# Kernel optimization log

Measured on AMD Instinct MI355X. Metric: run time of the kernel, lower is better.

The kernel has to match this reference:

```python
import jax, jax.numpy as jnp
import numpy as np

DIM = 1024
N_HEADS = 16
HEAD_DIM = DIM // N_HEADS


def setup_inputs() -> dict:
    key = jax.random.key(0)
    ks = jax.random.split(key, 6)
    s = DIM ** -0.5
    return {
        "x": jax.random.normal(ks[0], (2, 2048, DIM), dtype=jnp.float32),
        "Wq": jax.random.normal(ks[1], (DIM, DIM), dtype=jnp.float32) * s,
        "Wk": jax.random.normal(ks[2], (DIM, DIM), dtype=jnp.float32) * s,
        "Wv": jax.random.normal(ks[3], (DIM, DIM), dtype=jnp.float32) * s,
        "Wo": jax.random.normal(ks[4], (DIM, DIM), dtype=jnp.float32) * s,
        "bo": jax.random.normal(ks[5], (DIM,), dtype=jnp.float32) * 0.01,
    }


def reference(x, Wq, Wk, Wv, Wo, bo):
    B, T, C = x.shape
    H, D = N_HEADS, HEAD_DIM
    # Linear(dim, dim, bias=False): y = x @ W^T
    q = (x @ Wq.T).reshape(B, T, H, D).transpose(0, 2, 1, 3)  # B H T D
    k = (x @ Wk.T).reshape(B, T, H, D).transpose(0, 2, 1, 3)
    v = (x @ Wv.T).reshape(B, T, H, D).transpose(0, 2, 1, 3)
    q = q * (D ** -0.5)
    attn = jnp.einsum('bhqd,bhkd->bhqk', q, k)  # B H T T
    causal_mask = jnp.triu(jnp.ones((T, T), dtype=bool), k=1)
    attn = jnp.where(causal_mask, -jnp.inf, attn)
    attn = jax.nn.softmax(attn, axis=-1)
    out = jnp.einsum('bhqk,bhkd->bhqd', attn, v)  # B H T D
    out = out.transpose(0, 2, 1, 3).reshape(B, T, C)
    return out @ Wo.T + bo
```

## Files before the change

kernel.cpp:

```cpp
#include <hip/hip_runtime.h>
#include <math.h>

typedef __attribute__((ext_vector_type(8))) short bf16x8;
typedef __attribute__((ext_vector_type(4))) float f32x4;
typedef __attribute__((ext_vector_type(16))) float f32x16;

__device__ __forceinline__ ushort f2bf(float f) {
  union { float f; unsigned u; } v; v.f = f;
  return (ushort)((v.u + 0x8000u) >> 16);
}

__device__ __forceinline__ void g2l16(const void* g, void* l) {
  __builtin_amdgcn_global_load_lds((const __attribute__((address_space(1))) unsigned*)g,
                                   (__attribute__((address_space(3))) unsigned*)l, 16, 0, 0);
}

__global__ __launch_bounds__(256) void cast_all(const float* __restrict__ x,
                                                const float* __restrict__ Wq,
                                                const float* __restrict__ Wk,
                                                const float* __restrict__ Wv,
                                                const float* __restrict__ Wo,
                                                ushort* __restrict__ xbf,
                                                ushort* __restrict__ wcat,
                                                float4* __restrict__ O32) {
  int i = blockIdx.x * 256 + threadIdx.x;
  if (i < 1048576) {
    float4 v = ((const float4*)x)[i];
    ushort4 u; u.x = f2bf(v.x); u.y = f2bf(v.y); u.z = f2bf(v.z); u.w = f2bf(v.w);
    ((ushort4*)xbf)[i] = u;
  } else if (i < 2097152) {
    int j = i - 1048576;
    int sel = j >> 18;
    const float* src = (sel == 0) ? Wq : (sel == 1) ? Wk : (sel == 2) ? Wv : Wo;
    float scale = (sel == 0) ? 0.125f * 1.44269504088896f : 1.0f;
    float4 v = ((const float4*)src)[j & 0x3FFFF];
    ushort4 u;
    u.x = f2bf(v.x * scale); u.y = f2bf(v.y * scale);
    u.z = f2bf(v.z * scale); u.w = f2bf(v.w * scale);
    ((ushort4*)wcat)[j] = u;
  } else {
    O32[i - 2097152] = float4{0.f, 0.f, 0.f, 0.f};
  }
}

__global__ __launch_bounds__(256) void gemm_qkv(const ushort* __restrict__ A,
                                                const ushort* __restrict__ B,
                                                ushort* __restrict__ C3,
                                                ushort* __restrict__ Vt) {
  const int K = 1024;
  __shared__ __align__(16) ushort smem[17408];
  ushort* As = smem;
  ushort* Bs = smem + 8192;
  const int m0 = blockIdx.y * 128, n0 = blockIdx.x * 128;
  const int tid = threadIdx.x, lane = tid & 63, wid = tid >> 6;
  const int quad = lane >> 4, lc = lane & 15;
  const int lrow = lane >> 2, lcol = (lane & 3) * 8;
  const int wm = (wid >> 1) * 64, wn = (wid & 1) * 64;

  f32x4 acc[4][4] = {};

  auto stage = [&](int k0, int nb) {
    const ushort* Ag = A + (size_t)(m0 + wid * 32 + lrow) * K + k0 + lcol;
    g2l16(Ag, &As[nb * 4096 + wid * 1024]);
    g2l16(Ag + (size_t)16 * K, &As[nb * 4096 + wid * 1024 + 512]);
    const ushort* Bg = B + (size_t)(n0 + wid * 32 + lrow) * K + k0 + lcol;
    g2l16(Bg, &Bs[nb * 4096 + wid * 1024]);
    g2l16(Bg + (size_t)16 * K, &Bs[nb * 4096 + wid * 1024 + 512]);
  };

  stage(0, 0);
  for (int k0 = 0; k0 < K; k0 += 32) {
    const int nb = (k0 >> 5) & 1;
    __syncthreads();
    if (k0 + 32 < K) stage(k0 + 32, nb ^ 1);

    bf16x8 af[4], bfr[4];
#pragma unroll
    for (int t = 0; t < 4; t++)
      af[t] = *(const bf16x8*)&As[nb * 4096 + (wm + t * 16 + lc) * 32 + quad * 8];
#pragma unroll
    for (int t = 0; t < 4; t++)
      bfr[t] = *(const bf16x8*)&Bs[nb * 4096 + (wn + t * 16 + lc) * 32 + quad * 8];
#pragma unroll
    for (int mt = 0; mt < 4; mt++)
#pragma unroll
      for (int nt = 0; nt < 4; nt++)
        acc[mt][nt] = __builtin_amdgcn_mfma_f32_16x16x32_bf16(af[mt], bfr[nt], acc[mt][nt], 0, 0, 0);
  }

  const int sel = n0 >> 10;
  if (sel < 2) {
#pragma unroll
    for (int mt = 0; mt < 4; mt++) {
#pragma unroll
      for (int r = 0; r < 4; r++) {
        int row = m0 + wm + mt * 16 + quad * 4 + r;
#pragma unroll
        for (int nt = 0; nt < 4; nt++) {
          int col = n0 + wn + nt * 16 + lc;
          size_t dst = ((size_t)sel << 22) + (size_t)row * 1024 + (col & 1023);
          C3[dst] = f2bf(acc[mt][nt][r]);
        }
      }
    }
  } else {
    __syncthreads();
#pragma unroll
    for (int mt = 0; mt < 4; mt++)
#pragma unroll
      for (int r = 0; r < 4; r++) {
        int tl = wm + mt * 16 + quad * 4 + r;
#pragma unroll
        for (int nt = 0; nt < 4; nt++)
          smem[(wn + nt * 16 + lc) * 136 + tl] = f2bf(acc[mt][nt][r]);
      }
    __syncthreads();
    const int hd0 = n0 - 2048, b = m0 >> 11, t_base = m0 & 2047;
#pragma unroll
    for (int i = 0; i < 8; i++) {
      int idx = i * 256 + tid;
      int dl = idx >> 4, tc = (idx & 15) * 8;
      uint4 v = *(const uint4*)&smem[dl * 136 + tc];
      int hd = hd0 + dl;
      *(uint4*)(Vt + (size_t)(b * 16 + (hd >> 6)) * 131072 +
                (size_t)(hd & 63) * 2048 + t_base + tc) = v;
    }
  }
}

__global__ __launch_bounds__(256) void gemm_proj(const ushort* __restrict__ A,
                                                 const ushort* __restrict__ B,
                                                 float* __restrict__ C,
                                                 const float* __restrict__ bias) {
  const int K = 1024;
  __shared__ __align__(16) ushort As[2][2][128 * 32];
  __shared__ __align__(16) ushort Bs[2][2][64 * 32];
  const int m0 = blockIdx.y * 128, n0 = blockIdx.x * 64;
  const int tid = threadIdx.x, lane = tid & 63, wid = tid >> 6;
  const int quad = lane >> 4, lc = lane & 15;
  const int lrow = lane >> 2, lcol = (lane & 3) * 8;
  const int wm = (wid >> 1) * 64, wn = (wid & 1) * 32;

  f32x4 acc[4][2] = {};

  auto stage = [&](int k0, int nb) {
    const ushort* Ag = A + (size_t)(m0 + wid * 32 + lrow) * K + k0 + lcol;
    g2l16(Ag,                       &As[nb][0][wid * 1024]);
    g2l16(Ag + (size_t)16 * K,      &As[nb][0][wid * 1024 + 512]);
    g2l16(Ag + 32,                  &As[nb][1][wid * 1024]);
    g2l16(Ag + (size_t)16 * K + 32, &As[nb][1][wid * 1024 + 512]);
    const ushort* Bg = B + (size_t)(n0 + wid * 16 + lrow) * K + k0 + lcol;
    g2l16(Bg,      &Bs[nb][0][wid * 512]);
    g2l16(Bg + 32, &Bs[nb][1][wid * 512]);
  };

  stage(0, 0);
  for (int k0 = 0; k0 < K; k0 += 64) {
    const int nb = (k0 >> 6) & 1;
    __syncthreads();
    if (k0 + 64 < K) stage(k0 + 64, nb ^ 1);

#pragma unroll
    for (int ks = 0; ks < 2; ks++) {
      bf16x8 af[4], bfr[2];
#pragma unroll
      for (int t = 0; t < 4; t++)
        af[t] = *(const bf16x8*)&As[nb][ks][(wm + t * 16 + lc) * 32 + quad * 8];
#pragma unroll
      for (int t = 0; t < 2; t++)
        bfr[t] = *(const bf16x8*)&Bs[nb][ks][(wn + t * 16 + lc) * 32 + quad * 8];
#pragma unroll
      for (int mt = 0; mt < 4; mt++)
#pragma unroll
        for (int nt = 0; nt < 2; nt++)
          acc[mt][nt] = __builtin_amdgcn_mfma_f32_16x16x32_bf16(af[mt], bfr[nt], acc[mt][nt], 0, 0, 0);
    }
  }

#pragma unroll
  for (int mt = 0; mt < 4; mt++) {
#pragma unroll
    for (int r = 0; r < 4; r++) {
      int row = m0 + wm + mt * 16 + quad * 4 + r;
#pragma unroll
      for (int nt = 0; nt < 2; nt++) {
        int col = n0 + wn + nt * 16 + lc;
        C[(size_t)row * 1024 + col] = acc[mt][nt][r] + bias[col];
      }
    }
  }
}

__global__ __launch_bounds__(256, 3) void attn_kernel(const ushort* __restrict__ Qb,
                                                      const ushort* __restrict__ Kb,
                                                      const ushort* __restrict__ Vt,
                                                      float* __restrict__ O32,
                                                      float* __restrict__ L32) {
  __shared__ __align__(16) ushort Ks[3][4096];
  __shared__ __align__(16) ushort Vs[3][4096];

  const int bh = blockIdx.x, b = bh >> 4, h = bh & 15;
  const int f = (int)blockIdx.y;
  int qi, ci;
  if (f < 16)      { qi = 12 + (f >> 2); ci = f & 3; }
  else if (f < 28) { int g = f - 16; int q3 = g / 3; qi = 8 + q3; ci = g - 3 * q3; }
  else if (f < 36) { int g = f - 28; qi = 4 + (g >> 1); ci = g & 1; }
  else             { qi = f - 36; ci = 0; }
  const int t0 = ci * 8;
  const int t1 = min(t0 + 8, 2 * qi + 2);

  const int tid = threadIdx.x, lane = tid & 63, wid = tid >> 6;
  const int hi = lane >> 5, ln = lane & 31;
  const int qbw = qi * 128 + wid * 32;
  const int qg = qbw + ln;

  const size_t kbase = (size_t)(b * 2048) * 1024 + h * 64;
  const size_t vbase = (size_t)bh * 131072;

  bf16x8 qf[4];
  {
    const ushort* Qp = Qb + kbase + (size_t)qg * 1024 + hi * 8;
#pragma unroll
    for (int dc = 0; dc < 4; dc++)
      qf[dc] = *(const bf16x8*)(Qp + dc * 16);
  }
  asm volatile("" :: "v"(qf[0]), "v"(qf[1]), "v"(qf[2]), "v"(qf[3]));

  f32x16 o_acc[2] = {};
  float l_own = 0.f;

  const int krow = lane >> 3, kcol = lane & 7;
  const int dsw = (kcol ^ krow) << 3;

  auto stage = [&](int kb, int nb) {
    const ushort* gK = Kb + kbase + (size_t)(kb + wid * 8 + krow) * 1024 + dsw;
    g2l16(gK, &Ks[nb][wid * 512]);
    g2l16(gK + (size_t)32 * 1024, &Ks[nb][2048 + wid * 512]);
    const ushort* gV = Vt + vbase + (size_t)(wid * 8 + krow) * 2048 + kb + dsw;
    g2l16(gV, &Vs[nb][wid * 512]);
    g2l16(gV + (size_t)32 * 2048, &Vs[nb][2048 + wid * 512]);
  };

  const int sx = ln & 7;

  stage(t0 * 64, 0);
  if (t0 + 1 < t1) stage(t0 * 64 + 64, 1);
  int nb = 0;
  for (int kt = t0; kt < t1; kt++) {
    const int kb = kt * 64;
    if (kt + 1 < t1) asm volatile("s_waitcnt vmcnt(4)" ::: "memory");
    else             asm volatile("s_waitcnt vmcnt(0)" ::: "memory");
    __builtin_amdgcn_s_barrier();
    __builtin_amdgcn_sched_barrier(0);
    if (kt + 2 < t1) {
      int sb = (nb >= 1) ? nb - 1 : 2;
      stage(kb + 128, sb);
    }

    if (kb <= qbw + 31) {
      const ushort* ks = &Ks[nb][0];
      const ushort* vs = &Vs[nb][0];

      unsigned pa[4][4];
#pragma unroll
      for (int g64 = 0; g64 < 2; g64++) {
        f32x16 s;
#pragma unroll
        for (int z = 0; z < 16; z++) s[z] = 0.f;
        __builtin_amdgcn_s_setprio(1);
#pragma unroll
        for (int dc = 0; dc < 4; dc++) {
          bf16x8 kf = *(const bf16x8*)&ks[(g64 * 32 + ln) * 64 + (((dc * 2 + hi) ^ sx) << 3)];
          s = __builtin_amdgcn_mfma_f32_32x32x16_bf16(kf, qf[dc], s, 0, 0, 0);
        }
        __builtin_amdgcn_s_setprio(0);
        const bool dmask = (kb + g64 * 32 + 31 > qbw);
        unsigned U[8];
#pragma unroll
        for (int g = 0; g < 4; g++) {
          float e[4];
#pragma unroll
          for (int j = 0; j < 4; j++) {
            float sv = s[g * 4 + j];
            if (dmask && (kb + g64 * 32 + g * 8 + hi * 4 + j > qg)) sv = -1e30f;
            e[j] = __builtin_amdgcn_exp2f(sv);
          }
          l_own += (e[0] + e[1]) + (e[2] + e[3]);
          ushort b0 = f2bf(e[0]), b1 = f2bf(e[1]), b2 = f2bf(e[2]), b3 = f2bf(e[3]);
          U[g * 2]     = (unsigned)b0 | ((unsigned)b1 << 16);
          U[g * 2 + 1] = (unsigned)b2 | ((unsigned)b3 << 16);
        }
#pragma unroll
        for (int half = 0; half < 2; half++)
#pragma unroll
          for (int w = 0; w < 4; w++)
            pa[g64 * 2 + half][w] = U[half * 4 + w];
      }

      __builtin_amdgcn_s_setprio(1);
#pragma unroll
      for (int m = 0; m < 4; m++) {
        bf16x8 pfrag;
#pragma unroll
        for (int w = 0; w < 4; w++) ((unsigned*)&pfrag)[w] = pa[m][w];
#pragma unroll
        for (int dg = 0; dg < 2; dg++) {
          const ushort* vrow = &vs[(dg * 32 + ln) * 64];
          bf16x8 vbf;
          *(unsigned long long*)&vbf =
              *(const unsigned long long*)&vrow[(((2 * m) ^ sx) << 3) + 4 * hi];
          *((unsigned long long*)&vbf + 1) =
              *(const unsigned long long*)&vrow[(((2 * m + 1) ^ sx) << 3) + 4 * hi];
          o_acc[dg] = __builtin_amdgcn_mfma_f32_32x32x16_bf16(pfrag, vbf, o_acc[dg], 0, 0, 0);
        }
      }
      __builtin_amdgcn_s_setprio(0);
    }
    nb = (nb == 2) ? 0 : nb + 1;
  }

  {
    float lt = l_own + __shfl_xor(l_own, 32);
    if (hi == 0) atomicAdd(&L32[(size_t)bh * 2048 + qg], lt);
  }
#pragma unroll
  for (int r = 0; r < 16; r++) {
    int q = qbw + (r & 3) + ((r >> 2) << 3) + hi * 4;
    size_t orow = ((size_t)(b * 2048) + q) * 1024 + h * 64 + ln;
    atomicAdd(&O32[orow], o_acc[0][r]);
    atomicAdd(&O32[orow + 32], o_acc[1][r]);
  }
}

__global__ __launch_bounds__(256) void normalize_kernel(const float* __restrict__ O32,
                                                        const float* __restrict__ L32,
                                                        ushort* __restrict__ Out) {
  const int row = blockIdx.x;
  const int tid = threadIdx.x;
  const int col = tid * 4;
  const int b = row >> 11, t = row & 2047, h = col >> 6;
  const float inv = 1.0f / L32[(size_t)(b * 16 + h) * 2048 + t];
  float4 o = ((const float4*)(O32 + (size_t)row * 1024))[tid];
  ushort4 u;
  u.x = f2bf(o.x * inv); u.y = f2bf(o.y * inv);
  u.z = f2bf(o.z * inv); u.w = f2bf(o.w * inv);
  ((ushort4*)(Out + (size_t)row * 1024))[tid] = u;
}

extern "C" void kernel_launch(void* const* d_in, const int* in_sizes, int n_in,
                              void* d_out, int out_size, void* d_ws, size_t ws_size,
                              hipStream_t stream) {
  const float* x  = (const float*)d_in[0];
  const float* Wq = (const float*)d_in[1];
  const float* Wk = (const float*)d_in[2];
  const float* Wv = (const float*)d_in[3];
  const float* Wo = (const float*)d_in[4];
  const float* bo = (const float*)d_in[5];
  float* out = (float*)d_out;

  char* ws = (char*)d_ws;
  ushort* xbf  = (ushort*)(ws);
  ushort* wcat = (ushort*)(ws + (8ull  << 20));
  ushort* qkv  = (ushort*)(ws + (16ull << 20));
  ushort* Qp   = qkv;
  ushort* Kp   = qkv + (1ull << 22);
  ushort* Vt   = qkv + (2ull << 22);
  float*  L32  = (float*)ws;
  float*  O32  = out;
  ushort* attn_out = Qp;

  cast_all<<<12288, 256, 0, stream>>>(x, Wq, Wk, Wv, Wo, xbf, wcat, (float4*)O32);

  gemm_qkv<<<dim3(24, 32), 256, 0, stream>>>(xbf, wcat, qkv, Vt);

  hipMemsetAsync(L32, 0, (size_t)32 * 2048 * 4, stream);

  attn_kernel<<<dim3(32, 40), 256, 0, stream>>>(Qp, Kp, Vt, O32, L32);

  normalize_kernel<<<4096, 256, 0, stream>>>(O32, L32, attn_out);

  gemm_proj<<<dim3(16, 32), 256, 0, stream>>>(
      attn_out, wcat + (size_t)3072 * 1024, out, bo);
}
```

Before: 199.5 us.

## Shrink attention blocks to two waves with single-buffered KV staging

Each attention block is cut from four waves covering 128 queries to two waves covering 64 queries, and the grid is doubled. The causal work split is now computed with a loop over query tiles. The triple-buffered async K/V pipeline is replaced by a single buffer loaded synchronously, with one wave staging K and the other V. Fully masked 32-key sub-tiles are skipped, unmasked tiles get a mask-free exp path, and bf16 packing uses perm. The aim is more blocks per CU and less masking work, at the cost of losing load/compute overlap and reusing each K/V tile across fewer queries.

```diff
diff --git a/kernel.cpp b/kernel.cpp
--- a/kernel.cpp
+++ b/kernel.cpp
@@ -191,27 +191,24 @@
   }
 }
 
-__global__ __launch_bounds__(256, 3) void attn_kernel(const ushort* __restrict__ Qb,
+__global__ __launch_bounds__(128, 5) void attn_kernel(const ushort* __restrict__ Qb,
                                                       const ushort* __restrict__ Kb,
                                                       const ushort* __restrict__ Vt,
                                                       float* __restrict__ O32,
                                                       float* __restrict__ L32) {
-  __shared__ __align__(16) ushort Ks[3][4096];
-  __shared__ __align__(16) ushort Vs[3][4096];
+  __shared__ __align__(16) ushort Ks[4096];
+  __shared__ __align__(16) ushort Vs[4096];
 
   const int bh = blockIdx.x, b = bh >> 4, h = bh & 15;
-  const int f = (int)blockIdx.y;
-  int qi, ci;
-  if (f < 16)      { qi = 12 + (f >> 2); ci = f & 3; }
-  else if (f < 28) { int g = f - 16; int q3 = g / 3; qi = 8 + q3; ci = g - 3 * q3; }
-  else if (f < 36) { int g = f - 28; qi = 4 + (g >> 1); ci = g & 1; }
-  else             { qi = f - 36; ci = 0; }
+  int rem = (int)blockIdx.y, qi2 = 31;
+  while (true) { int c = (qi2 + 8) >> 3; if (rem < c) break; rem -= c; qi2--; }
+  const int ci = rem;
   const int t0 = ci * 8;
-  const int t1 = min(t0 + 8, 2 * qi + 2);
+  const int t1 = min(t0 + 8, qi2 + 1);
 
   const int tid = threadIdx.x, lane = tid & 63, wid = tid >> 6;
   const int hi = lane >> 5, ln = lane & 31;
-  const int qbw = qi * 128 + wid * 32;
+  const int qbw = qi2 * 64 + wid * 32;
   const int qg = qbw + ln;
 
   const size_t kbase = (size_t)(b * 2048) * 1024 + h * 64;
@@ -224,7 +221,6 @@
     for (int dc = 0; dc < 4; dc++)
       qf[dc] = *(const bf16x8*)(Qp + dc * 16);
   }
-  asm volatile("" :: "v"(qf[0]), "v"(qf[1]), "v"(qf[2]), "v"(qf[3]));
 
   f32x16 o_acc[2] = {};
   float l_own = 0.f;
@@ -232,80 +228,85 @@
   const int krow = lane >> 3, kcol = lane & 7;
   const int dsw = (kcol ^ krow) << 3;
 
-  auto stage = [&](int kb, int nb) {
-    const ushort* gK = Kb + kbase + (size_t)(kb + wid * 8 + krow) * 1024 + dsw;
-    g2l16(gK, &Ks[nb][wid * 512]);
-    g2l16(gK + (size_t)32 * 1024, &Ks[nb][2048 + wid * 512]);
-    const ushort* gV = Vt + vbase + (size_t)(wid * 8 + krow) * 2048 + kb + dsw;
-    g2l16(gV, &Vs[nb][wid * 512]);
-    g2l16(gV + (size_t)32 * 2048, &Vs[nb][2048 + wid * 512]);
+  auto stage = [&](int kb) {
+    if (wid == 0) {
+      const ushort* gK = Kb + kbase + (size_t)(kb + krow) * 1024 + dsw;
+#pragma unroll
+      for (int i = 0; i < 8; i++)
+        g2l16(gK + (size_t)(i * 8) * 1024, &Ks[i * 512]);
+    } else {
+      const ushort* gV = Vt + vbase + (size_t)krow * 2048 + kb + dsw;
+#pragma unroll
+      for (int i = 0; i < 8; i++)
+        g2l16(gV + (size_t)(i * 8) * 2048, &Vs[i * 512]);
+    }
   };
 
   const int sx = ln & 7;
 
-  stage(t0 * 64, 0);
-  if (t0 + 1 < t1) stage(t0 * 64 + 64, 1);
-  int nb = 0;
   for (int kt = t0; kt < t1; kt++) {
     const int kb = kt * 64;
-    if (kt + 1 < t1) asm volatile("s_waitcnt vmcnt(4)" ::: "memory");
-    else             asm volatile("s_waitcnt vmcnt(0)" ::: "memory");
     __builtin_amdgcn_s_barrier();
-    __builtin_amdgcn_sched_barrier(0);
-    if (kt + 2 < t1) {
-      int sb = (nb >= 1) ? nb - 1 : 2;
-      stage(kb + 128, sb);
-    }
-
-    if (kb <= qbw + 31) {
-      const ushort* ks = &Ks[nb][0];
-      const ushort* vs = &Vs[nb][0];
-
-      unsigned pa[4][4];
-#pragma unroll
-      for (int g64 = 0; g64 < 2; g64++) {
-        f32x16 s;
-#pragma unroll
-        for (int z = 0; z < 16; z++) s[z] = 0.f;
-        __builtin_amdgcn_s_setprio(1);
-#pragma unroll
-        for (int dc = 0; dc < 4; dc++) {
-          bf16x8 kf = *(const bf16x8*)&ks[(g64 * 32 + ln) * 64 + (((dc * 2 + hi) ^ sx) << 3)];
-          s = __builtin_amdgcn_mfma_f32_32x32x16_bf16(kf, qf[dc], s, 0, 0, 0);
-        }
-        __builtin_amdgcn_s_setprio(0);
-        const bool dmask = (kb + g64 * 32 + 31 > qbw);
-        unsigned U[8];
+    stage(kb);
+    asm volatile("s_waitcnt vmcnt(0)" ::: "memory");
+    __builtin_amdgcn_s_barrier();
+
+#pragma unroll
+    for (int g64 = 0; g64 < 2; g64++) {
+      if (kb + g64 * 32 > qbw + 31) continue;
+      f32x16 s;
+#pragma unroll
+      for (int z = 0; z < 16; z++) s[z] = 0.f;
+      __builtin_amdgcn_s_setprio(1);
+#pragma unroll
+      for (int dc = 0; dc < 4; dc++) {
+        bf16x8 kf = *(const bf16x8*)&Ks[(g64 * 32 + ln) * 64 + (((dc * 2 + hi) ^ sx) << 3)];
+        s = __builtin_amdgcn_mfma_f32_32x32x16_bf16(kf, qf[dc], s, 0, 0, 0);
+      }
+      __builtin_amdgcn_s_setprio(0);
+
+      unsigned U[8];
+      const bool dmask = (kb + g64 * 32 + 31 > qbw);
+      if (dmask) {
+        const int c = qg - kb - g64 * 32 - hi * 4;
 #pragma unroll
         for (int g = 0; g < 4; g++) {
           float e[4];
 #pragma unroll
           for (int j = 0; j < 4; j++) {
             float sv = s[g * 4 + j];
-            if (dmask && (kb + g64 * 32 + g * 8 + hi * 4 + j > qg)) sv = -1e30f;
+            if (g * 8 + j > c) sv = -1e30f;
             e[j] = __builtin_amdgcn_exp2f(sv);
           }
           l_own += (e[0] + e[1]) + (e[2] + e[3]);
-          ushort b0 = f2bf(e[0]), b1 = f2bf(e[1]), b2 = f2bf(e[2]), b3 = f2bf(e[3]);
-          U[g * 2]     = (unsigned)b0 | ((unsigned)b1 << 16);
-          U[g * 2 + 1] = (unsigned)b2 | ((unsigned)b3 << 16);
+          union { float f; unsigned u; } f0{e[0]}, f1{e[1]}, f2{e[2]}, f3{e[3]};
+          U[g * 2]     = __builtin_amdgcn_perm(f1.u + 0x8000u, f0.u + 0x8000u, 0x07060302u);
+          U[g * 2 + 1] = __builtin_amdgcn_perm(f3.u + 0x8000u, f2.u + 0x8000u, 0x07060302u);
         }
-#pragma unroll
-        for (int half = 0; half < 2; half++)
-#pragma unroll
-          for (int w = 0; w < 4; w++)
-            pa[g64 * 2 + half][w] = U[half * 4 + w];
+      } else {
+#pragma unroll
+        for (int g = 0; g < 4; g++) {
+          float e[4];
+#pragma unroll
+          for (int j = 0; j < 4; j++)
+            e[j] = __builtin_amdgcn_exp2f(s[g * 4 + j]);
+          l_own += (e[0] + e[1]) + (e[2] + e[3]);
+          union { float f; unsigned u; } f0{e[0]}, f1{e[1]}, f2{e[2]}, f3{e[3]};
+          U[g * 2]     = __builtin_amdgcn_perm(f1.u + 0x8000u, f0.u + 0x8000u, 0x07060302u);
+          U[g * 2 + 1] = __builtin_amdgcn_perm(f3.u + 0x8000u, f2.u + 0x8000u, 0x07060302u);
+        }
       }
 
       __builtin_amdgcn_s_setprio(1);
 #pragma unroll
-      for (int m = 0; m < 4; m++) {
+      for (int half = 0; half < 2; half++) {
+        const int m = g64 * 2 + half;
         bf16x8 pfrag;
 #pragma unroll
-        for (int w = 0; w < 4; w++) ((unsigned*)&pfrag)[w] = pa[m][w];
+        for (int w = 0; w < 4; w++) ((unsigned*)&pfrag)[w] = U[half * 4 + w];
 #pragma unroll
         for (int dg = 0; dg < 2; dg++) {
-          const ushort* vrow = &vs[(dg * 32 + ln) * 64];
+          const ushort* vrow = &Vs[(dg * 32 + ln) * 64];
           bf16x8 vbf;
           *(unsigned long long*)&vbf =
               *(const unsigned long long*)&vrow[(((2 * m) ^ sx) << 3) + 4 * hi];
@@ -316,7 +317,6 @@
       }
       __builtin_amdgcn_s_setprio(0);
     }
-    nb = (nb == 2) ? 0 : nb + 1;
   }
 
   {
@@ -375,7 +375,7 @@
 
   hipMemsetAsync(L32, 0, (size_t)32 * 2048 * 4, stream);
 
-  attn_kernel<<<dim3(32, 40), 256, 0, stream>>>(Qp, Kp, Vt, O32, L32);
+  attn_kernel<<<dim3(32, 80), 128, 0, stream>>>(Qp, Kp, Vt, O32, L32);
 
   normalize_kernel<<<4096, 256, 0, stream>>>(O32, L32, attn_out);
 
```

New measurement: 203.4 us. About the same (+2.0%).
